# Kernel tuning notes

Measured on AMD Instinct MI355X. Metric: run time of the kernel, lower is better.

The kernel has to match this reference:

```python
import jax, jax.numpy as jnp
import numpy as np

INPUT_DIM = 1024
EMBED_DIMS = 128


def setup_inputs() -> dict:
    key = jax.random.key(0)
    ks = jax.random.split(key, 7)
    s_in = 1.0 / np.sqrt(INPUT_DIM)
    x = jax.random.normal(ks[0], (4, 4096, INPUT_DIM), dtype=jnp.float32)
    Wq = jax.random.uniform(ks[1], (INPUT_DIM, EMBED_DIMS), jnp.float32, -s_in, s_in)
    bq = jax.random.uniform(ks[2], (EMBED_DIMS,), jnp.float32, -s_in, s_in)
    Wk = jax.random.uniform(ks[3], (INPUT_DIM, EMBED_DIMS), jnp.float32, -s_in, s_in)
    bk = jax.random.uniform(ks[4], (EMBED_DIMS,), jnp.float32, -s_in, s_in)
    Wv = jax.random.uniform(ks[5], (INPUT_DIM, EMBED_DIMS), jnp.float32, -s_in, s_in)
    bv = jax.random.uniform(ks[6], (EMBED_DIMS,), jnp.float32, -s_in, s_in)
    return {"x": x, "Wq": Wq, "bq": bq, "Wk": Wk, "bk": bk, "Wv": Wv, "bv": bv}


def reference(x, Wq, bq, Wk, bk, Wv, bv):
    # x: [B, L, C]
    Q = jnp.einsum('blc,cd->bld', x, Wq) + bq  # [B, L, D]
    K = jnp.einsum('blc,cd->bld', x, Wk) + bk
    V = jnp.einsum('blc,cd->bld', x, Wv) + bv
    d_k = Q.shape[-1]
    scores = jnp.einsum('bld,bmd->blm', Q, K) / jnp.sqrt(jnp.float32(d_k))  # [B, L, L]
    attn = jax.nn.softmax(scores, axis=-1)
    return jnp.einsum('blm,bmd->bld', attn, V)  # [B, L, D]
```

## Files before the change

### kernel.cpp

```cpp
#include <hip/hip_runtime.h>
#include <stdint.h>

typedef __bf16 bf16;
typedef __bf16 bf16x8 __attribute__((ext_vector_type(8)));
typedef __bf16 bf16x4 __attribute__((ext_vector_type(4)));
typedef _Float16 f16;
typedef f16 f16x8 __attribute__((ext_vector_type(8)));
typedef f16 f16x4 __attribute__((ext_vector_type(4)));
typedef f16 f16x2 __attribute__((ext_vector_type(2)));
typedef float f32x4 __attribute__((ext_vector_type(4)));
typedef float f32x16 __attribute__((ext_vector_type(16)));
typedef uint32_t u32x4 __attribute__((ext_vector_type(4)));

#define LQ    16384
#define CDIM  1024
#define DDIM  128
#define NSPLIT 4
#define QS 0.12751741f

static __device__ __forceinline__ uint32_t pkrtz(float a, float b) {
  return __builtin_bit_cast(uint32_t, __builtin_amdgcn_cvt_pkrtz(a, b));
}

__global__ void prep_kernel(const float* __restrict__ Wq, const float* __restrict__ Wk,
                            const float* __restrict__ Wv, const float* __restrict__ bq,
                            const float* __restrict__ bk, const float* __restrict__ bv,
                            bf16* __restrict__ Wt, float* __restrict__ bias_all) {
  int idx = blockIdx.x * 256 + threadIdx.x;
  int p = idx >> 17;
  int rem = idx & 131071;
  int k = rem >> 7, n = rem & 127;
  const float* W = (p == 0) ? Wq : (p == 1) ? Wk : Wv;
  float s = (p == 0) ? QS : 1.0f;
  Wt[(size_t)(p * 128 + n) * CDIM + k] = (bf16)(W[rem] * s);
  if (idx < 384) {
    int pp = idx >> 7, nn = idx & 127;
    const float* b = (pp == 0) ? bq : (pp == 1) ? bk : bv;
    bias_all[idx] = b[nn] * ((pp == 0) ? QS : 1.0f);
  }
}

__global__ __launch_bounds__(256, 3) void qkv_gemm(
    const float* __restrict__ x, const bf16* __restrict__ Wt,
    const float* __restrict__ bias_all,
    bf16* __restrict__ Qw, bf16* __restrict__ Kw, f16* __restrict__ Vtw) {
  __shared__ bf16 As[2][128 * 64];
  __shared__ bf16 Bs[2][64 * 64];
  const int t = threadIdx.x;
  const int w = t >> 6;
  const int lane = t & 63;
  const int l31 = lane & 31;
  const int hi = lane >> 5;
  const int lin = blockIdx.x;
  const int logical = (lin & 7) * 96 + (lin >> 3);
  const int mi = logical / 6;
  const int rr = logical % 6;
  const int y = rr >> 1;
  const int nb = rr & 1;
  const int m0 = mi * 128;
  const int n0 = nb * 64;
  const bf16* W = Wt + (size_t)y * (DDIM * CDIM) + (size_t)n0 * CDIM;
  const int m_off = (w & 1) * 64;
  const int n_off = (w >> 1) * 32;

  const f32x16 z16 = {0.f,0.f,0.f,0.f,0.f,0.f,0.f,0.f,0.f,0.f,0.f,0.f,0.f,0.f,0.f,0.f};
  f32x16 acc[2];
  acc[0] = z16; acc[1] = z16;

  const int srow = t >> 3;
  const int g = t & 7;
  const int sg = (g ^ (srow & 7)) * 8;
  const int scol = g * 8;

  float4 xa[4][2];
  bf16x8 wa[2];
#pragma unroll
  for (int c = 0; c < 4; c++) {
    const float* p = &x[(size_t)(m0 + c * 32 + srow) * CDIM + scol];
    xa[c][0] = *(const float4*)p;
    xa[c][1] = *(const float4*)(p + 4);
  }
#pragma unroll
  for (int c = 0; c < 2; c++)
    wa[c] = *(const bf16x8*)&W[(size_t)(c * 32 + srow) * CDIM + scol];

  for (int kc = 0; kc < 16; kc++) {
    bf16* Ab = As[kc & 1];
    bf16* Bb = Bs[kc & 1];
#pragma unroll
    for (int c = 0; c < 4; c++) {
      bf16x8 v;
      v[0] = (bf16)xa[c][0].x; v[1] = (bf16)xa[c][0].y;
      v[2] = (bf16)xa[c][0].z; v[3] = (bf16)xa[c][0].w;
      v[4] = (bf16)xa[c][1].x; v[5] = (bf16)xa[c][1].y;
      v[6] = (bf16)xa[c][1].z; v[7] = (bf16)xa[c][1].w;
      *(bf16x8*)&Ab[(c * 32 + srow) * 64 + sg] = v;
    }
#pragma unroll
    for (int c = 0; c < 2; c++)
      *(bf16x8*)&Bb[(c * 32 + srow) * 64 + sg] = wa[c];

    const int kn = (kc < 15 ? kc + 1 : 15) * 64;
#pragma unroll
    for (int c = 0; c < 4; c++) {
      const float* p = &x[(size_t)(m0 + c * 32 + srow) * CDIM + kn + scol];
      xa[c][0] = *(const float4*)p;
      xa[c][1] = *(const float4*)(p + 4);
    }
#pragma unroll
    for (int c = 0; c < 2; c++)
      wa[c] = *(const bf16x8*)&W[(size_t)(c * 32 + srow) * CDIM + kn + scol];

    __syncthreads();

#pragma unroll
    for (int ks = 0; ks < 4; ks++) {
      const int rg = ((ks * 2 + hi) ^ (l31 & 7)) * 8;
      bf16x8 bfr = *(const bf16x8*)&Bb[(n_off + l31) * 64 + rg];
      bf16x8 af0 = *(const bf16x8*)&Ab[(m_off + l31) * 64 + rg];
      bf16x8 af1 = *(const bf16x8*)&Ab[(m_off + 32 + l31) * 64 + rg];
      acc[0] = __builtin_amdgcn_mfma_f32_32x32x16_bf16(af0, bfr, acc[0], 0, 0, 0);
      acc[1] = __builtin_amdgcn_mfma_f32_32x32x16_bf16(af1, bfr, acc[1], 0, 0, 0);
    }
  }

  const float bias = bias_all[y * 128 + n0 + n_off + l31];
  const int n = n0 + n_off + l31;

  if (y < 2) {
    bf16* outp = (y == 0) ? Qw : Kw;
#pragma unroll
    for (int mt = 0; mt < 2; mt++)
#pragma unroll
      for (int r = 0; r < 16; r++) {
        int m = m0 + m_off + mt * 32 + (r & 3) + 8 * (r >> 2) + 4 * hi;
        outp[(size_t)m * DDIM + n] = (bf16)(acc[mt][r] + bias);
      }
  } else {
#pragma unroll
    for (int mt = 0; mt < 2; mt++)
#pragma unroll
      for (int gq = 0; gq < 4; gq++) {
        int mbase = m0 + m_off + mt * 32 + 8 * gq + 4 * hi;
        f16x4 pv;
#pragma unroll
        for (int r = 0; r < 4; r++) pv[r] = (f16)(acc[mt][gq * 4 + r] + bias);
        *(f16x4*)&Vtw[(size_t)n * LQ + mbase] = pv;
      }
  }
}

__global__ __launch_bounds__(256, 2) void flash_kernel(
    const bf16* __restrict__ Qw, const bf16* __restrict__ Kw, const f16* __restrict__ Vtw,
    bf16* __restrict__ Opb, float* __restrict__ lp) {
  __shared__ bf16 Kl[2][64 * 136];
  __shared__ f16  Vl[2][128 * 72];

  const int t = threadIdx.x;
  const int w = t >> 6;
  const int lane = t & 63;
  const int l31 = lane & 31;
  const int hi = lane >> 5;
  const int lin = blockIdx.y * 128 + blockIdx.x;
  const int logical = ((lin & 7) << 6) + (lin >> 3);
  const int qb = logical & 127;
  const int sp = logical >> 7;
  const int batch = qb >> 5;
  const int q0w = qb * 128 + w * 32;
  const int kv_base = batch * 4096 + sp * 1024;

  bf16x8 qf[8];
#pragma unroll
  for (int ks = 0; ks < 8; ks++)
    qf[ks] = *(const bf16x8*)&Qw[(size_t)(q0w + l31) * DDIM + ks * 16 + hi * 8];

  const f32x16 z16 = {0.f,0.f,0.f,0.f,0.f,0.f,0.f,0.f,0.f,0.f,0.f,0.f,0.f,0.f,0.f,0.f};
  f32x16 o[4];
  o[0] = z16; o[1] = z16; o[2] = z16; o[3] = z16;
  f32x16 liacc = z16;

  f16x8 ones;
#pragma unroll
  for (int i = 0; i < 8; i++) ones[i] = (f16)1.f;

  const int kr = t >> 4;
  const int kcol = (t & 15) << 3;
  const int vr = t >> 3;
  const int vcol = (t & 7) << 3;

  bf16x8 ka[4];
  f16x8 va[4];
#pragma unroll
  for (int c = 0; c < 4; c++)
    ka[c] = *(const bf16x8*)&Kw[(size_t)(kv_base + c * 16 + kr) * DDIM + kcol];
#pragma unroll
  for (int c = 0; c < 4; c++)
    va[c] = *(const f16x8*)&Vtw[(size_t)(c * 32 + vr) * LQ + kv_base + vcol];

  for (int tile = 0; tile < 16; tile++) {
    bf16* Kb = Kl[tile & 1];
    f16*  Vb = Vl[tile & 1];
#pragma unroll
    for (int c = 0; c < 4; c++)
      *(bf16x8*)&Kb[(c * 16 + kr) * 136 + kcol] = ka[c];
#pragma unroll
    for (int c = 0; c < 4; c++)
      *(f16x8*)&Vb[(c * 32 + vr) * 72 + vcol] = va[c];

    const int kvn = kv_base + (tile < 15 ? tile + 1 : 15) * 64;
#pragma unroll
    for (int c = 0; c < 4; c++)
      ka[c] = *(const bf16x8*)&Kw[(size_t)(kvn + c * 16 + kr) * DDIM + kcol];
#pragma unroll
    for (int c = 0; c < 4; c++)
      va[c] = *(const f16x8*)&Vtw[(size_t)(c * 32 + vr) * LQ + kvn + vcol];

    __syncthreads();

    f32x16 sv0 = z16, sv1 = z16;
    __builtin_amdgcn_s_setprio(1);
#pragma unroll
    for (int ks = 0; ks < 8; ks++) {
      bf16x8 kf0 = *(const bf16x8*)&Kb[l31 * 136 + ks * 16 + hi * 8];
      bf16x8 kf1 = *(const bf16x8*)&Kb[(32 + l31) * 136 + ks * 16 + hi * 8];
      sv0 = __builtin_amdgcn_mfma_f32_32x32x16_bf16(kf0, qf[ks], sv0, 0, 0, 0);
      sv1 = __builtin_amdgcn_mfma_f32_32x32x16_bf16(kf1, qf[ks], sv1, 0, 0, 0);
    }
    __builtin_amdgcn_s_setprio(0);

#pragma unroll
    for (int r = 0; r < 16; r++) {
      sv0[r] = __builtin_amdgcn_exp2f(sv0[r]);
      sv1[r] = __builtin_amdgcn_exp2f(sv1[r]);
    }

#pragma unroll
    for (int mk = 0; mk < 2; mk++) {
      const f32x16 s = mk ? sv1 : sv0;
#pragma unroll
      for (int h = 0; h < 2; h++) {
        const int b = h * 8;
        uint32_t a0 = pkrtz(s[b + 0], s[b + 1]);
        uint32_t a1 = pkrtz(s[b + 2], s[b + 3]);
        uint32_t a2 = pkrtz(s[b + 4], s[b + 5]);
        uint32_t a3 = pkrtz(s[b + 6], s[b + 7]);
        asm("v_permlane32_swap_b32 %0, %1" : "+v"(a0), "+v"(a2));
        asm("v_permlane32_swap_b32 %0, %1" : "+v"(a1), "+v"(a3));
        u32x4 aw; aw.x = a0; aw.y = a1; aw.z = a2; aw.w = a3;
        f16x8 pa = __builtin_bit_cast(f16x8, aw);
        __builtin_amdgcn_s_setprio(1);
#pragma unroll
        for (int dt = 0; dt < 4; dt++) {
          f16x8 vf = *(const f16x8*)&Vb[(dt * 32 + l31) * 72 + mk * 32 + h * 16 + hi * 8];
          o[dt] = __builtin_amdgcn_mfma_f32_32x32x16_f16(pa, vf, o[dt], 0, 0, 0);
        }
        liacc = __builtin_amdgcn_mfma_f32_32x32x16_f16(pa, ones, liacc, 0, 0, 0);
        __builtin_amdgcn_s_setprio(0);
      }
    }
  }

  const size_t po = (size_t)sp * LQ * DDIM;
#pragma unroll
  for (int dt = 0; dt < 4; dt++)
#pragma unroll
    for (int r = 0; r < 16; r++) {
      int q = q0w + (r & 3) + 8 * (r >> 2) + 4 * hi;
      Opb[po + (size_t)q * DDIM + dt * 32 + l31] = (bf16)o[dt][r];
    }
  if (l31 == 0) {
#pragma unroll
    for (int r = 0; r < 16; r++)
      lp[(size_t)sp * LQ + q0w + (r & 3) + 8 * (r >> 2) + 4 * hi] = liacc[r];
  }
}

__global__ void combine_kernel(const bf16* __restrict__ Opb, const float* __restrict__ lp,
                               float* __restrict__ out) {
  int idx = blockIdx.x * 256 + threadIdx.x;
  int q = idx >> 5;
  int d = (idx & 31) * 4;
  float lsum = 0.f;
  float acc[4] = {0.f, 0.f, 0.f, 0.f};
#pragma unroll
  for (int sp = 0; sp < NSPLIT; sp++) {
    lsum += lp[(size_t)sp * LQ + q];
    bf16x4 ov = *(const bf16x4*)&Opb[(size_t)sp * LQ * DDIM + (size_t)q * DDIM + d];
#pragma unroll
    for (int j = 0; j < 4; j++) acc[j] += (float)ov[j];
  }
  float inv = 1.0f / lsum;
  float4 r;
  r.x = acc[0] * inv; r.y = acc[1] * inv; r.z = acc[2] * inv; r.w = acc[3] * inv;
  *(float4*)&out[(size_t)q * DDIM + d] = r;
}

extern "C" void kernel_launch(void* const* d_in, const int* in_sizes, int n_in,
                              void* d_out, int out_size, void* d_ws, size_t ws_size,
                              hipStream_t stream) {
  const float* x  = (const float*)d_in[0];
  const float* Wq = (const float*)d_in[1];
  const float* bq = (const float*)d_in[2];
  const float* Wk = (const float*)d_in[3];
  const float* bk = (const float*)d_in[4];
  const float* Wv = (const float*)d_in[5];
  const float* bv = (const float*)d_in[6];
  char* ws = (char*)d_ws;
  bf16* Qw   = (bf16*)(ws);
  bf16* Kw   = (bf16*)(ws + ((size_t)4 << 20));
  f16*  Vtw  = (f16*)(ws + ((size_t)8 << 20));
  bf16* Wt   = (bf16*)(ws + ((size_t)12 << 20));
  float* bias_all = (float*)(ws + ((size_t)12 << 20) + 786432);
  bf16* Opb  = (bf16*)(ws + ((size_t)13 << 20));
  float* lpp = (float*)(ws + ((size_t)29 << 20));
  float* out = (float*)d_out;

  prep_kernel<<<1536, 256, 0, stream>>>(Wq, Wk, Wv, bq, bk, bv, Wt, bias_all);
  qkv_gemm<<<768, 256, 0, stream>>>(x, Wt, bias_all, Qw, Kw, Vtw);
  flash_kernel<<<dim3(128, NSPLIT), 256, 0, stream>>>(Qw, Kw, Vtw, Opb, lpp);
  combine_kernel<<<2048, 256, 0, stream>>>(Opb, lpp, out);
}
```

Baseline: 184.7 us.

## Retile QKV GEMM so each block computes all three projections for 64 rows

```diff
diff --git a/kernel.cpp b/kernel.cpp
--- a/kernel.cpp
+++ b/kernel.cpp
@@ -7,7 +7,6 @@
 typedef _Float16 f16;
 typedef f16 f16x8 __attribute__((ext_vector_type(8)));
 typedef f16 f16x4 __attribute__((ext_vector_type(4)));
-typedef f16 f16x2 __attribute__((ext_vector_type(2)));
 typedef float f32x4 __attribute__((ext_vector_type(4)));
 typedef float f32x16 __attribute__((ext_vector_type(16)));
 typedef uint32_t u32x4 __attribute__((ext_vector_type(4)));
@@ -20,6 +19,11 @@
 
 static __device__ __forceinline__ uint32_t pkrtz(float a, float b) {
   return __builtin_bit_cast(uint32_t, __builtin_amdgcn_cvt_pkrtz(a, b));
+}
+
+static __device__ __forceinline__ void lds_barrier() {
+  asm volatile("s_waitcnt lgkmcnt(0)" ::: "memory");
+  __builtin_amdgcn_s_barrier();
 }
 
 __global__ void prep_kernel(const float* __restrict__ Wq, const float* __restrict__ Wk,
@@ -40,113 +44,101 @@
   }
 }
 
-__global__ __launch_bounds__(256, 3) void qkv_gemm(
+__global__ __launch_bounds__(512, 1) void qkv_gemm(
     const float* __restrict__ x, const bf16* __restrict__ Wt,
     const float* __restrict__ bias_all,
     bf16* __restrict__ Qw, bf16* __restrict__ Kw, f16* __restrict__ Vtw) {
-  __shared__ bf16 As[2][128 * 64];
-  __shared__ bf16 Bs[2][64 * 64];
+  __shared__ bf16 As[2][64 * 64];
+  __shared__ bf16 Bs[2][384 * 64];
   const int t = threadIdx.x;
   const int w = t >> 6;
   const int lane = t & 63;
   const int l31 = lane & 31;
   const int hi = lane >> 5;
-  const int lin = blockIdx.x;
-  const int logical = (lin & 7) * 96 + (lin >> 3);
-  const int mi = logical / 6;
-  const int rr = logical % 6;
-  const int y = rr >> 1;
-  const int nb = rr & 1;
-  const int m0 = mi * 128;
-  const int n0 = nb * 64;
-  const bf16* W = Wt + (size_t)y * (DDIM * CDIM) + (size_t)n0 * CDIM;
-  const int m_off = (w & 1) * 64;
-  const int n_off = (w >> 1) * 32;
+  const int m0 = blockIdx.x * 64;
+  const int m_off = (w & 1) * 32;
+  const int n_off = ((w >> 1) & 3) * 32;
 
   const f32x16 z16 = {0.f,0.f,0.f,0.f,0.f,0.f,0.f,0.f,0.f,0.f,0.f,0.f,0.f,0.f,0.f,0.f};
-  f32x16 acc[2];
-  acc[0] = z16; acc[1] = z16;
+  f32x16 acc[3];
+  acc[0] = z16; acc[1] = z16; acc[2] = z16;
 
   const int srow = t >> 3;
   const int g = t & 7;
-  const int sg = (g ^ (srow & 7)) * 8;
+  const int sgoff = (g ^ (srow & 7)) * 8;
   const int scol = g * 8;
 
-  float4 xa[4][2];
-  bf16x8 wa[2];
-#pragma unroll
-  for (int c = 0; c < 4; c++) {
-    const float* p = &x[(size_t)(m0 + c * 32 + srow) * CDIM + scol];
-    xa[c][0] = *(const float4*)p;
-    xa[c][1] = *(const float4*)(p + 4);
-  }
-#pragma unroll
-  for (int c = 0; c < 2; c++)
-    wa[c] = *(const bf16x8*)&W[(size_t)(c * 32 + srow) * CDIM + scol];
+  float4 xa[2];
+  bf16x8 wa[6];
+  {
+    const float* p = &x[(size_t)(m0 + srow) * CDIM + scol];
+    xa[0] = *(const float4*)p;
+    xa[1] = *(const float4*)(p + 4);
+  }
+#pragma unroll
+  for (int c = 0; c < 6; c++)
+    wa[c] = *(const bf16x8*)&Wt[(size_t)(c * 64 + srow) * CDIM + scol];
 
   for (int kc = 0; kc < 16; kc++) {
     bf16* Ab = As[kc & 1];
     bf16* Bb = Bs[kc & 1];
-#pragma unroll
-    for (int c = 0; c < 4; c++) {
+    {
       bf16x8 v;
-      v[0] = (bf16)xa[c][0].x; v[1] = (bf16)xa[c][0].y;
-      v[2] = (bf16)xa[c][0].z; v[3] = (bf16)xa[c][0].w;
-      v[4] = (bf16)xa[c][1].x; v[5] = (bf16)xa[c][1].y;
-      v[6] = (bf16)xa[c][1].z; v[7] = (bf16)xa[c][1].w;
-      *(bf16x8*)&Ab[(c * 32 + srow) * 64 + sg] = v;
-    }
-#pragma unroll
-    for (int c = 0; c < 2; c++)
-      *(bf16x8*)&Bb[(c * 32 + srow) * 64 + sg] = wa[c];
+      v[0] = (bf16)xa[0].x; v[1] = (bf16)xa[0].y;
+      v[2] = (bf16)xa[0].z; v[3] = (bf16)xa[0].w;
+      v[4] = (bf16)xa[1].x; v[5] = (bf16)xa[1].y;
+      v[6] = (bf16)xa[1].z; v[7] = (bf16)xa[1].w;
+      *(bf16x8*)&Ab[srow * 64 + sgoff] = v;
+    }
+#pragma unroll
+    for (int c = 0; c < 6; c++)
+      *(bf16x8*)&Bb[(c * 64 + srow) * 64 + sgoff] = wa[c];
 
     const int kn = (kc < 15 ? kc + 1 : 15) * 64;
-#pragma unroll
-    for (int c = 0; c < 4; c++) {
-      const float* p = &x[(size_t)(m0 + c * 32 + srow) * CDIM + kn + scol];
-      xa[c][0] = *(const float4*)p;
-      xa[c][1] = *(const float4*)(p + 4);
-    }
-#pragma unroll
-    for (int c = 0; c < 2; c++)
-      wa[c] = *(const bf16x8*)&W[(size_t)(c * 32 + srow) * CDIM + kn + scol];
-
-    __syncthreads();
+    {
+      const float* p = &x[(size_t)(m0 + srow) * CDIM + kn + scol];
+      xa[0] = *(const float4*)p;
+      xa[1] = *(const float4*)(p + 4);
+    }
+#pragma unroll
+    for (int c = 0; c < 6; c++)
+      wa[c] = *(const bf16x8*)&Wt[(size_t)(c * 64 + srow) * CDIM + kn + scol];
+
+    lds_barrier();
 
 #pragma unroll
     for (int ks = 0; ks < 4; ks++) {
       const int rg = ((ks * 2 + hi) ^ (l31 & 7)) * 8;
-      bf16x8 bfr = *(const bf16x8*)&Bb[(n_off + l31) * 64 + rg];
-      bf16x8 af0 = *(const bf16x8*)&Ab[(m_off + l31) * 64 + rg];
-      bf16x8 af1 = *(const bf16x8*)&Ab[(m_off + 32 + l31) * 64 + rg];
-      acc[0] = __builtin_amdgcn_mfma_f32_32x32x16_bf16(af0, bfr, acc[0], 0, 0, 0);
-      acc[1] = __builtin_amdgcn_mfma_f32_32x32x16_bf16(af1, bfr, acc[1], 0, 0, 0);
-    }
-  }
-
-  const float bias = bias_all[y * 128 + n0 + n_off + l31];
-  const int n = n0 + n_off + l31;
-
-  if (y < 2) {
-    bf16* outp = (y == 0) ? Qw : Kw;
-#pragma unroll
-    for (int mt = 0; mt < 2; mt++)
+      bf16x8 af = *(const bf16x8*)&Ab[(m_off + l31) * 64 + rg];
+#pragma unroll
+      for (int p = 0; p < 3; p++) {
+        bf16x8 bfr = *(const bf16x8*)&Bb[(p * 128 + n_off + l31) * 64 + rg];
+        acc[p] = __builtin_amdgcn_mfma_f32_32x32x16_bf16(af, bfr, acc[p], 0, 0, 0);
+      }
+    }
+  }
+
+  const int n = n_off + l31;
+#pragma unroll
+  for (int p = 0; p < 3; p++) {
+    const float bias = bias_all[p * 128 + n];
+    if (p < 2) {
+      bf16* outp = (p == 0) ? Qw : Kw;
 #pragma unroll
       for (int r = 0; r < 16; r++) {
-        int m = m0 + m_off + mt * 32 + (r & 3) + 8 * (r >> 2) + 4 * hi;
-        outp[(size_t)m * DDIM + n] = (bf16)(acc[mt][r] + bias);
+        int m = m0 + m_off + (r & 3) + 8 * (r >> 2) + 4 * hi;
+        outp[(size_t)m * DDIM + n] = (bf16)(acc[p][r] + bias);
       }
-  } else {
-#pragma unroll
-    for (int mt = 0; mt < 2; mt++)
+    } else {
 #pragma unroll
       for (int gq = 0; gq < 4; gq++) {
-        int mbase = m0 + m_off + mt * 32 + 8 * gq + 4 * hi;
+        int mbase = m0 + m_off + 8 * gq + 4 * hi;
         f16x4 pv;
 #pragma unroll
-        for (int r = 0; r < 4; r++) pv[r] = (f16)(acc[mt][gq * 4 + r] + bias);
+        for (int r = 0; r < 4; r++) pv[r] = (f16)(acc[p][gq * 4 + r] + bias);
         *(f16x4*)&Vtw[(size_t)n * LQ + mbase] = pv;
       }
+    }
   }
 }
 
@@ -215,7 +207,7 @@
     for (int c = 0; c < 4; c++)
       va[c] = *(const f16x8*)&Vtw[(size_t)(c * 32 + vr) * LQ + kvn + vcol];
 
-    __syncthreads();
+    lds_barrier();
 
     f32x16 sv0 = z16, sv1 = z16;
     __builtin_amdgcn_s_setprio(1);
@@ -316,7 +308,7 @@
   float* out = (float*)d_out;
 
   prep_kernel<<<1536, 256, 0, stream>>>(Wq, Wk, Wv, bq, bk, bv, Wt, bias_all);
-  qkv_gemm<<<768, 256, 0, stream>>>(x, Wt, bias_all, Qw, Kw, Vtw);
+  qkv_gemm<<<256, 512, 0, stream>>>(x, Wt, bias_all, Qw, Kw, Vtw);
   flash_kernel<<<dim3(128, NSPLIT), 256, 0, stream>>>(Qw, Kw, Vtw, Opb, lpp);
   combine_kernel<<<2048, 256, 0, stream>>>(Opb, lpp, out);
 }
```

Measured after the change: 171.2 us. 1.08x faster.
